# Kernel tuning notes

Measured on AMD Instinct MI355X. Metric: run time of the kernel, lower is better.

## Reference

```python
import jax, jax.numpy as jnp
import numpy as np

D_MODEL, D_STATE, D_CONV, EXPAND, L = 512, 16, 4, 2, 2048
D_INNER = EXPAND * D_MODEL


def _dwconv_causal(x, w, b):
    # x: (L, D), w: (D, K), b: (D,). torch Conv1d(groups=D, padding=K-1)[..., :L]
    K = w.shape[1]
    xp = jnp.pad(x, ((K - 1, 0), (0, 0)))
    windows = jnp.stack([xp[k:k + x.shape[0]] for k in range(K)], axis=-1)  # (L, D, K)
    return jnp.einsum('ldk,dk->ld', windows, w) + b


def _ssm_dir(x, inW, inb, cw, cb, xpW, xpb, dtW, dtb, outW, outb, A_log, Dp):
    xz = x @ inW + inb                      # (L, 2*Di)
    x_ssm, z = xz[:, :D_INNER], xz[:, D_INNER:]
    x_ssm = _dwconv_causal(x_ssm, cw, cb)   # (L, Di)
    sp = jax.nn.silu(x_ssm) @ xpW + xpb     # (L, Di + 2*S)
    delta = sp[:, :D_INNER]
    B = sp[:, D_INNER:D_INNER + D_STATE]
    C = sp[:, D_INNER + D_STATE:]
    dt = jax.nn.softplus(delta @ dtW + dtb)  # (L, Di)
    A = -jnp.exp(A_log)                      # (Di, S)
    dA = jnp.exp(dt[:, :, None] * A[None])                      # (L, Di, S)
    dBu = dt[:, :, None] * B[:, None, :] * x_ssm[:, :, None]    # (L, Di, S)

    def step(h, inp):
        a, bu = inp
        h = a * h + bu
        return h, h

    h0 = jnp.zeros((D_INNER, D_STATE), x.dtype)
    _, hs = jax.lax.scan(step, h0, (dA, dBu))   # (L, Di, S)
    y = jnp.einsum('lds,ls->ld', hs, C) + Dp * x_ssm
    return (y * jax.nn.silu(z)) @ outW + outb


def _make_params(key):
    ks = jax.random.split(key, 32)
    i = iter(range(32))
    def w(shape, scale=0.02):
        return (jax.random.normal(ks[next(i)], shape, jnp.float32) * scale)
    p = {}
    for pre in ('fwd_', 'bwd_'):
        p[pre + 'in_W'] = w((D_MODEL, 2 * D_INNER))
        p[pre + 'in_b'] = w((2 * D_INNER,))
        p[pre + 'conv_w'] = w((D_INNER, D_CONV), 0.1)
        p[pre + 'conv_b'] = w((D_INNER,))
        p[pre + 'xp_W'] = w((D_INNER, D_INNER + 2 * D_STATE))
        p[pre + 'xp_b'] = w((D_INNER + 2 * D_STATE,))
        p[pre + 'dt_W'] = w((D_INNER, D_INNER))
        p[pre + 'dt_b'] = w((D_INNER,))
        p[pre + 'out_W'] = w((D_INNER, D_MODEL))
        p[pre + 'out_b'] = w((D_MODEL,))
    p['A_log'] = jax.random.normal(ks[next(i)], (D_INNER, D_STATE), jnp.float32) * 0.5
    p['D_param'] = jnp.ones((D_INNER,), jnp.float32)
    p['fusion_W'] = w((2 * D_MODEL, D_MODEL))
    p['fusion_b'] = w((D_MODEL,))
    return p


def setup_inputs() -> dict:
    key = jax.random.key(0)
    kx, kp = jax.random.split(key)
    inp = {'x': jax.random.normal(kx, (L, D_MODEL), jnp.float32)}
    inp.update(_make_params(kp))
    return inp


def reference(x,
              fwd_in_W, fwd_in_b, fwd_conv_w, fwd_conv_b, fwd_xp_W, fwd_xp_b,
              fwd_dt_W, fwd_dt_b, fwd_out_W, fwd_out_b,
              bwd_in_W, bwd_in_b, bwd_conv_w, bwd_conv_b, bwd_xp_W, bwd_xp_b,
              bwd_dt_W, bwd_dt_b, bwd_out_W, bwd_out_b,
              A_log, D_param, fusion_W, fusion_b):
    out_fwd = _ssm_dir(x, fwd_in_W, fwd_in_b, fwd_conv_w, fwd_conv_b,
                       fwd_xp_W, fwd_xp_b, fwd_dt_W, fwd_dt_b,
                       fwd_out_W, fwd_out_b, A_log, D_param)
    out_bwd = _ssm_dir(x[::-1], bwd_in_W, bwd_in_b, bwd_conv_w, bwd_conv_b,
                       bwd_xp_W, bwd_xp_b, bwd_dt_W, bwd_dt_b,
                       bwd_out_W, bwd_out_b, A_log, D_param)[::-1]
    return jnp.concatenate([out_fwd, out_bwd], axis=-1) @ fusion_W + fusion_b
```

## Files before the change

### kernel.cpp

```cpp
#include <hip/hip_runtime.h>
#include <cmath>

#define L_SEQ 2048
#define DM 512
#define DI 1024
#define DS 16
#define NSP 1056
#define NC 64
#define CL 32

typedef unsigned short ushortT;
typedef unsigned int u32;
typedef __attribute__((ext_vector_type(8))) short short8;
typedef __attribute__((ext_vector_type(4))) float float4_t;
typedef __attribute__((address_space(1))) u32 gu32;
typedef __attribute__((address_space(3))) u32 lu32;

__device__ __forceinline__ float sigm(float x) { return 1.0f / (1.0f + __expf(-x)); }

__device__ __forceinline__ ushortT f2bf(float f) {
    unsigned u = __float_as_uint(f);
    unsigned r = u + 0x7FFFu + ((u >> 16) & 1u);
    return (ushortT)(r >> 16);
}

__device__ __forceinline__ void gl2lds16(const ushortT* g, ushortT* l) {
    __builtin_amdgcn_global_load_lds((gu32*)g, (lu32*)l, 16, 0, 0);
}

struct WC {
    const float* src[11];
    ushortT* dst[11];
    int ss[11], soff[11], ds_[11], tN[11], mode[11];
    int off[12];
};

__global__ __launch_bounds__(256) void wcvt_all(WC wc)
{
    __shared__ ushortT t[32][33];
    int b = blockIdx.x;
    int m = 0;
    while (b >= wc.off[m + 1]) ++m;
    int tl = b - wc.off[m];
    int n0 = (tl % wc.tN[m]) * 32;
    int k0 = (tl / wc.tN[m]) * 32;
    const float* W = wc.src[m];
    ushortT* D = wc.dst[m];
    int ss = wc.ss[m], soff = wc.soff[m], ds = wc.ds_[m];
    int tx = threadIdx.x & 31, ty = threadIdx.x >> 5;
    if (wc.mode[m] == 1) {
        #pragma unroll
        for (int i = 0; i < 32; i += 8)
            D[(size_t)(k0 + ty + i) * ds + n0 + tx] =
                f2bf(W[(size_t)(k0 + ty + i) * ss + soff + n0 + tx]);
    } else {
        #pragma unroll
        for (int i = 0; i < 32; i += 8)
            t[ty + i][tx] = f2bf(W[(size_t)(k0 + ty + i) * ss + soff + n0 + tx]);
        __syncthreads();
        #pragma unroll
        for (int i = 0; i < 32; i += 8)
            D[(size_t)(n0 + ty + i) * ds + k0 + tx] = t[tx][ty + i];
    }
}

__global__ __launch_bounds__(256) void bias_fold(
    const float* __restrict__ xpb0, const float* __restrict__ xpb1,
    const float* __restrict__ dtW0, const float* __restrict__ dtW1,
    const float* __restrict__ dtb0, const float* __restrict__ dtb1,
    const float* __restrict__ outb0, const float* __restrict__ outb1,
    const float* __restrict__ fuW, const float* __restrict__ fub,
    float* __restrict__ BFdt0, float* __restrict__ BFdt1, float* __restrict__ BFof)
{
    __shared__ float red[256];
    int o = blockIdx.x;
    int tid = threadIdx.x;
    float acc = 0.0f;
    if (o < 2112) {
        int dir = o >= 1056;
        int m = o - dir * 1056;
        const float* xpb = dir ? xpb1 : xpb0;
        float* BF = dir ? BFdt1 : BFdt0;
        if (m >= 1024) {
            if (tid == 0) BF[m] = xpb[m];
            return;
        }
        const float* dtW = dir ? dtW1 : dtW0;
        const float* dtb = dir ? dtb1 : dtb0;
        for (int n = tid; n < 1024; n += 256) acc += xpb[n] * dtW[n * 1024 + m];
        red[tid] = acc;
        __syncthreads();
        for (int s = 128; s > 0; s >>= 1) {
            if (tid < s) red[tid] += red[tid + s];
            __syncthreads();
        }
        if (tid == 0) BF[m] = red[0] + dtb[m];
    } else {
        int n = o - 2112;
        for (int j = tid; j < 1024; j += 256) {
            float ob = (j < 512) ? outb0[j] : outb1[j - 512];
            acc += ob * fuW[(size_t)j * 512 + n];
        }
        red[tid] = acc;
        __syncthreads();
        for (int s = 128; s > 0; s >>= 1) {
            if (tid < s) red[tid] += red[tid + s];
            __syncthreads();
        }
        if (tid == 0) BFof[n] = red[0] + fub[n];
    }
}

__global__ __launch_bounds__(256) void xcvt_k(const float* __restrict__ x,
                                              ushortT* __restrict__ xb, int n)
{
    int i = (blockIdx.x * 256 + threadIdx.x) * 4;
    if (i < n) {
        float4_t v = *(const float4_t*)(x + i);
        xb[i + 0] = f2bf(v[0]); xb[i + 1] = f2bf(v[1]);
        xb[i + 2] = f2bf(v[2]); xb[i + 3] = f2bf(v[3]);
    }
}

template<int BM, int BN>
__global__ __launch_bounds__(256) void gemm_bf16(
    const ushortT* __restrict__ A, int lda, long long Astr, int revAmode,
    const ushortT* __restrict__ W, long long Wstr,
    const float* __restrict__ bias0, const float* __restrict__ bias1,
    float* __restrict__ Cf, int ldcf, long long Cfstr,
    float* __restrict__ Cf2, int ldcf2, long long Cf2str, int Nsplit,
    ushortT* __restrict__ Cb, int ldcb, long long Cbstr,
    int M, int N, int K, int epi)
{
    const int dir = blockIdx.z;
    A  += (size_t)dir * Astr;
    W  += (size_t)dir * Wstr;
    if (Cf)  Cf  += (size_t)dir * Cfstr;
    if (Cf2) Cf2 += (size_t)dir * Cf2str;
    if (Cb)  Cb  += (size_t)dir * Cbstr;
    const float* bias = dir ? bias1 : bias0;
    const int revA = (revAmode == 2) ? dir : revAmode;

    constexpr int BK = 64;
    constexpr int MI = BM / 32;
    constexpr int NI = BN / 32;
    constexpr int CA = BM / 32;
    constexpr int CB = BN / 32;

    __shared__ ushortT As[2][BM * BK];
    __shared__ ushortT Bs[2][BN * BK];

    const int tid  = threadIdx.x;
    const int wave = tid >> 6;
    const int lane = tid & 63;
    const int quad = lane >> 4;
    const int r    = lane & 15;
    const int wm   = (wave >> 1) * (BM / 2);
    const int wn   = (wave & 1) * (BN / 2);
    const int bm   = blockIdx.y * BM;
    const int bn   = blockIdx.x * BN;

    const int lrow = lane >> 3;
    const int lk   = (lane & 7) * 8;

    const ushortT* gA[CA];
    ushortT* lA[CA];
    #pragma unroll
    for (int c = 0; c < CA; ++c) {
        int row = bm + c * 32 + wave * 8 + lrow;
        if (revA) row = M - 1 - row;
        gA[c] = A + (size_t)row * lda + lk;
        lA[c] = &As[0][(c * 32 + wave * 8) * BK];
    }
    const ushortT* gB[CB];
    ushortT* lB[CB];
    #pragma unroll
    for (int c = 0; c < CB; ++c) {
        int row = bn + c * 32 + wave * 8 + lrow;
        if (row > N - 1) row = N - 1;
        gB[c] = W + (size_t)row * K + lk;
        lB[c] = &Bs[0][(c * 32 + wave * 8) * BK];
    }
    constexpr int ABUF = BM * BK;
    constexpr int BBUF = BN * BK;

    float4_t acc[MI][NI];
    #pragma unroll
    for (int i = 0; i < MI; ++i)
        #pragma unroll
        for (int j = 0; j < NI; ++j)
            acc[i][j] = (float4_t){0.f, 0.f, 0.f, 0.f};

    const int nsteps = K >> 6;

    #pragma unroll
    for (int c = 0; c < CA; ++c) gl2lds16(gA[c], lA[c]);
    #pragma unroll
    for (int c = 0; c < CB; ++c) gl2lds16(gB[c], lB[c]);

    for (int i = 0; i < nsteps; i += 2) {
        __syncthreads();
        {
            int kq = (i + 1) << 6;
            if (i + 1 < nsteps) {
                #pragma unroll
                for (int c = 0; c < CA; ++c) gl2lds16(gA[c] + kq, lA[c] + ABUF);
                #pragma unroll
                for (int c = 0; c < CB; ++c) gl2lds16(gB[c] + kq, lB[c] + BBUF);
            }
        }
        #pragma unroll
        for (int kh = 0; kh < 2; ++kh) {
            short8 af[MI], bf[NI];
            #pragma unroll
            for (int mi = 0; mi < MI; ++mi)
                af[mi] = *(const short8*)&As[0][(wm + mi * 16 + r) * BK + kh * 32 + quad * 8];
            #pragma unroll
            for (int ni = 0; ni < NI; ++ni)
                bf[ni] = *(const short8*)&Bs[0][(wn + ni * 16 + r) * BK + kh * 32 + quad * 8];
            #pragma unroll
            for (int mi = 0; mi < MI; ++mi)
                #pragma unroll
                for (int ni = 0; ni < NI; ++ni)
                    acc[mi][ni] = __builtin_amdgcn_mfma_f32_16x16x32_bf16(
                        af[mi], bf[ni], acc[mi][ni], 0, 0, 0);
        }
        __syncthreads();
        {
            int kq = (i + 2) << 6;
            if (i + 2 < nsteps) {
                #pragma unroll
                for (int c = 0; c < CA; ++c) gl2lds16(gA[c] + kq, lA[c]);
                #pragma unroll
                for (int c = 0; c < CB; ++c) gl2lds16(gB[c] + kq, lB[c]);
            }
        }
        #pragma unroll
        for (int kh = 0; kh < 2; ++kh) {
            short8 af[MI], bf[NI];
            #pragma unroll
            for (int mi = 0; mi < MI; ++mi)
                af[mi] = *(const short8*)&As[1][(wm + mi * 16 + r) * BK + kh * 32 + quad * 8];
            #pragma unroll
            for (int ni = 0; ni < NI; ++ni)
                bf[ni] = *(const short8*)&Bs[1][(wn + ni * 16 + r) * BK + kh * 32 + quad * 8];
            #pragma unroll
            for (int mi = 0; mi < MI; ++mi)
                #pragma unroll
                for (int ni = 0; ni < NI; ++ni)
                    acc[mi][ni] = __builtin_amdgcn_mfma_f32_16x16x32_bf16(
                        af[mi], bf[ni], acc[mi][ni], 0, 0, 0);
        }
    }

    #pragma unroll
    for (int mi = 0; mi < MI; ++mi) {
        int rowb = bm + wm + mi * 16 + quad * 4;
        #pragma unroll
        for (int ni = 0; ni < NI; ++ni) {
            int gn = bn + wn + ni * 16 + r;
            if (gn < N) {
                float bv = bias ? bias[gn] : 0.0f;
                #pragma unroll
                for (int j = 0; j < 4; ++j) {
                    int orow = rowb + j;
                    float v = acc[mi][ni][j] + bv;
                    if (epi == 1 && gn < Nsplit) v = (v > 20.0f) ? v : log1pf(__expf(v));
                    if (epi == 3) {
                        atomicAdd(&Cf[(size_t)orow * ldcf + gn], v);
                    } else {
                        if (gn < Nsplit) {
                            if (Cf) Cf[(size_t)orow * ldcf + gn] = v;
                        } else if (Cf2) {
                            Cf2[(size_t)orow * ldcf2 + gn - Nsplit] = v;
                        }
                        if (Cb) Cb[(size_t)orow * ldcb + gn] = f2bf(v);
                    }
                }
            }
        }
    }
}

__global__ __launch_bounds__(256) void conv_k(
    const float* __restrict__ XZ,
    const float* __restrict__ cw0, const float* __restrict__ cw1,
    const float* __restrict__ cb0, const float* __restrict__ cb1,
    float* __restrict__ XC, ushortT* __restrict__ SCb)
{
    int dir = blockIdx.z;
    XZ += (size_t)dir * L_SEQ * 2 * DI;
    XC += (size_t)dir * L_SEQ * DI;
    SCb += (size_t)dir * L_SEQ * DI;
    const float* cw = dir ? cw1 : cw0;
    const float* cb = dir ? cb1 : cb0;
    int idx = blockIdx.x * 256 + threadIdx.x;
    int d = idx & (DI - 1);
    int l = idx >> 10;
    float w0 = cw[d * 4 + 0], w1 = cw[d * 4 + 1], w2 = cw[d * 4 + 2], w3 = cw[d * 4 + 3];
    float acc = cb[d];
    if (l >= 3) acc += XZ[(size_t)(l - 3) * (2 * DI) + d] * w0;
    if (l >= 2) acc += XZ[(size_t)(l - 2) * (2 * DI) + d] * w1;
    if (l >= 1) acc += XZ[(size_t)(l - 1) * (2 * DI) + d] * w2;
    acc += XZ[(size_t)l * (2 * DI) + d] * w3;
    XC[idx] = acc;
    SCb[idx] = f2bf(acc * sigm(acc));
}

__global__ __launch_bounds__(256) void scanA_k(
    const float* __restrict__ DT, const float* __restrict__ XC,
    const float* __restrict__ BC, const float* __restrict__ Alog,
    float* __restrict__ Pend, float* __restrict__ Hl)
{
    __shared__ float Bsh[CL][DS];
    int dir = blockIdx.z;
    int c = blockIdx.y;
    int d = blockIdx.x * 256 + threadIdx.x;
    DT += (size_t)dir * L_SEQ * DI;
    XC += (size_t)dir * L_SEQ * DI;
    BC += (size_t)dir * L_SEQ * 32;
    int l0 = c * CL;
    for (int i = threadIdx.x; i < CL * DS; i += 256) {
        int ll = i >> 4, ss = i & 15;
        Bsh[ll][ss] = BC[(size_t)(l0 + ll) * 32 + ss];
    }
    __syncthreads();
    float Ae[DS], h[DS], P[DS];
    #pragma unroll
    for (int s = 0; s < DS; ++s) { Ae[s] = -__expf(Alog[d * DS + s]); h[s] = 0.f; P[s] = 1.f; }
    for (int t = 0; t < CL; ++t) {
        int l = l0 + t;
        float dt = DT[(size_t)l * DI + d];
        float xv = XC[(size_t)l * DI + d];
        float dtx = dt * xv;
        #pragma unroll
        for (int s = 0; s < DS; ++s) {
            float e = __expf(dt * Ae[s]);
            h[s] = e * h[s] + dtx * Bsh[t][s];
            P[s] *= e;
        }
    }
    size_t o = ((size_t)(dir * NC + c) * DI + d) * DS;
    #pragma unroll
    for (int s = 0; s < DS; ++s) { Pend[o + s] = P[s]; Hl[o + s] = h[s]; }
}

__global__ __launch_bounds__(256) void scanB_k(
    const float* __restrict__ Pend, const float* __restrict__ Hl, float* __restrict__ Hs)
{
    int idx = blockIdx.x * 256 + threadIdx.x;
    float h = 0.f;
    int ds = idx & 16383;
    int dir = idx >> 14;
    for (int c = 0; c < NC; ++c) {
        size_t o = ((size_t)(dir * NC + c)) * (DI * DS) + ds;
        Hs[o] = h;
        h = Pend[o] * h + Hl[o];
    }
}

__global__ __launch_bounds__(256) void scanC_k(
    const float* __restrict__ DT, const float* __restrict__ XC,
    const float* __restrict__ BC, const float* __restrict__ XZ,
    const float* __restrict__ Alog, const float* __restrict__ Dp,
    const float* __restrict__ Hs, ushortT* __restrict__ Gb)
{
    __shared__ float Bsh[CL][DS];
    __shared__ float Csh[CL][DS];
    int dir = blockIdx.z;
    int c = blockIdx.y;
    int d = blockIdx.x * 256 + threadIdx.x;
    DT += (size_t)dir * L_SEQ * DI;
    XC += (size_t)dir * L_SEQ * DI;
    BC += (size_t)dir * L_SEQ * 32;
    XZ += (size_t)dir * L_SEQ * (2 * DI);
    Gb += (size_t)dir * L_SEQ * DI;
    int l0 = c * CL;
    for (int i = threadIdx.x; i < CL * DS; i += 256) {
        int ll = i >> 4, ss = i & 15;
        size_t base = (size_t)(l0 + ll) * 32;
        Bsh[ll][ss] = BC[base + ss];
        Csh[ll][ss] = BC[base + DS + ss];
    }
    __syncthreads();
    float Ae[DS], h[DS];
    size_t o = ((size_t)(dir * NC + c) * DI + d) * DS;
    #pragma unroll
    for (int s = 0; s < DS; ++s) { Ae[s] = -__expf(Alog[d * DS + s]); h[s] = Hs[o + s]; }
    float dpv = Dp[d];
    for (int t = 0; t < CL; ++t) {
        int l = l0 + t;
        float dt = DT[(size_t)l * DI + d];
        float xv = XC[(size_t)l * DI + d];
        float dtx = dt * xv;
        float y = 0.f;
        #pragma unroll
        for (int s = 0; s < DS; ++s) {
            float e = __expf(dt * Ae[s]);
            h[s] = e * h[s] + dtx * Bsh[t][s];
            y += h[s] * Csh[t][s];
        }
        y += dpv * xv;
        float z = XZ[(size_t)l * (2 * DI) + DI + d];
        Gb[(size_t)l * DI + d] = f2bf(y * (z * sigm(z)));
    }
}

extern "C" void kernel_launch(void* const* d_in, const int* in_sizes, int n_in,
                              void* d_out, int out_size, void* d_ws, size_t ws_size,
                              hipStream_t stream)
{
    (void)in_sizes; (void)n_in; (void)out_size; (void)ws_size;
    const float* x = (const float*)d_in[0];
    const float* inW[2]  = {(const float*)d_in[1],  (const float*)d_in[11]};
    const float* inb[2]  = {(const float*)d_in[2],  (const float*)d_in[12]};
    const float* cw[2]   = {(const float*)d_in[3],  (const float*)d_in[13]};
    const float* cb[2]   = {(const float*)d_in[4],  (const float*)d_in[14]};
    const float* xpW[2]  = {(const float*)d_in[5],  (const float*)d_in[15]};
    const float* xpb[2]  = {(const float*)d_in[6],  (const float*)d_in[16]};
    const float* dtW[2]  = {(const float*)d_in[7],  (const float*)d_in[17]};
    const float* dtb[2]  = {(const float*)d_in[8],  (const float*)d_in[18]};
    const float* outW[2] = {(const float*)d_in[9],  (const float*)d_in[19]};
    const float* outb[2] = {(const float*)d_in[10], (const float*)d_in[20]};
    const float* Alog = (const float*)d_in[21];
    const float* Dp   = (const float*)d_in[22];
    const float* fuW  = (const float*)d_in[23];
    const float* fub  = (const float*)d_in[24];
    float* out = (float*)d_out;

    float* ws = (float*)d_ws;
    size_t off = 0;
    auto alloc = [&](size_t n) { float* p = ws + off; off += n; return p; };
    float* XZ   = alloc((size_t)2 * L_SEQ * 2 * DI);
    float* XC   = alloc((size_t)2 * L_SEQ * DI);
    float* DTb  = alloc((size_t)2 * L_SEQ * DI);
    float* BCf  = alloc((size_t)2 * L_SEQ * 32);
    float* Pend = alloc((size_t)2 * NC * DI * DS);
    float* Hl   = alloc((size_t)2 * NC * DI * DS);
    float* Hs   = alloc((size_t)2 * NC * DI * DS);
    float* BFdt0 = alloc(1056);
    float* BFdt1 = alloc(1056);
    float* BFof  = alloc(512);

    ushortT* wsu = (ushortT*)(ws + off);
    size_t uoff = 0;
    auto ualloc = [&](size_t n) { ushortT* p = wsu + uoff; uoff += n; return p; };
    ushortT* WtIn  = ualloc((size_t)2 * (2 * DI) * DM);
    ushortT* WtDt  = ualloc((size_t)2 * DI * DI);
    ushortT* WtFu  = ualloc((size_t)DM * DI);
    ushortT* WtXpF = ualloc((size_t)2 * NSP * DI);
    ushortT* XpD   = ualloc((size_t)2 * DI * DI);
    ushortT* OutC  = ualloc((size_t)2 * DI * DM);
    ushortT* WtOF  = ualloc((size_t)2 * DM * DI);
    ushortT* XB    = ualloc((size_t)L_SEQ * DM);
    ushortT* SCb   = ualloc((size_t)2 * L_SEQ * DI);
    ushortT* Gb    = ualloc((size_t)2 * L_SEQ * DI);

    dim3 blk(256);

    hipMemsetAsync(out, 0, (size_t)L_SEQ * DM * sizeof(float), stream);

    WC wc;
    struct E { const float* s; ushortT* d; int ss, so, ds, N, K, mode; };
    E es[11] = {
        {inW[0],  WtIn,                          2 * DI, 0,    DM, 2 * DI, DM, 0},
        {inW[1],  WtIn + (size_t)2 * DI * DM,    2 * DI, 0,    DM, 2 * DI, DM, 0},
        {dtW[0],  WtDt,                          DI,     0,    DI, DI,     DI, 0},
        {dtW[1],  WtDt + (size_t)DI * DI,        DI,     0,    DI, DI,     DI, 0},
        {fuW,     WtFu,                          DM,     0,    DI, DM,     DI, 0},
        {xpW[0],  WtXpF + (size_t)DI * DI,       NSP,    DI,   DI, 32,     DI, 0},
        {xpW[1],  WtXpF + (size_t)NSP * DI + (size_t)DI * DI, NSP, DI, DI, 32, DI, 0},
        {xpW[0],  XpD,                           NSP,    0,    DI, DI,     DI, 1},
        {xpW[1],  XpD + (size_t)DI * DI,         NSP,    0,    DI, DI,     DI, 1},
        {outW[0], OutC,                          DM,     0,    DM, DM,     DI, 1},
        {outW[1], OutC + (size_t)DI * DM,        DM,     0,    DM, DM,     DI, 1},
    };
    wc.off[0] = 0;
    for (int m = 0; m < 11; ++m) {
        wc.src[m] = es[m].s; wc.dst[m] = es[m].d;
        wc.ss[m] = es[m].ss; wc.soff[m] = es[m].so; wc.ds_[m] = es[m].ds;
        wc.tN[m] = es[m].N / 32; wc.mode[m] = es[m].mode;
        wc.off[m + 1] = wc.off[m] + (es[m].N / 32) * (es[m].K / 32);
    }
    wcvt_all<<<dim3(wc.off[11]), blk, 0, stream>>>(wc);
    xcvt_k<<<dim3(L_SEQ * DM / 1024), blk, 0, stream>>>(x, XB, L_SEQ * DM);
    bias_fold<<<dim3(2624), blk, 0, stream>>>(
        xpb[0], xpb[1], dtW[0], dtW[1], dtb[0], dtb[1],
        outb[0], outb[1], fuW, fub, BFdt0, BFdt1, BFof);

    gemm_bf16<64, 64><<<dim3(16, 16, 2), blk, 0, stream>>>(
        WtDt, DI, (long long)DI * DI, 0, XpD, (long long)DI * DI,
        nullptr, nullptr, nullptr, 0, 0, nullptr, 0, 0, DI,
        WtXpF, DI, (long long)NSP * DI, DI, DI, DI, 0);
    gemm_bf16<64, 64><<<dim3(16, 8, 2), blk, 0, stream>>>(
        WtFu, DI, (long long)DM, 0, OutC, (long long)DI * DM,
        nullptr, nullptr, nullptr, 0, 0, nullptr, 0, 0, DI,
        WtOF, DI, (long long)DM * DI, DM, DI, DM, 0);

    gemm_bf16<64, 128><<<dim3(16, 32, 2), blk, 0, stream>>>(
        XB, DM, 0, 2, WtIn, (long long)2 * DI * DM, inb[0], inb[1],
        XZ, 2 * DI, (long long)L_SEQ * 2 * DI, nullptr, 0, 0, 2 * DI,
        nullptr, 0, 0, L_SEQ, 2 * DI, DM, 0);
    conv_k<<<dim3(L_SEQ * DI / 256, 1, 2), blk, 0, stream>>>(
        XZ, cw[0], cw[1], cb[0], cb[1], XC, SCb);
    gemm_bf16<64, 64><<<dim3((NSP + 63) / 64, 32, 2), blk, 0, stream>>>(
        SCb, DI, (long long)L_SEQ * DI, 0, WtXpF, (long long)NSP * DI, BFdt0, BFdt1,
        DTb, DI, (long long)L_SEQ * DI, BCf, 32, (long long)L_SEQ * 32, DI,
        nullptr, 0, 0, L_SEQ, NSP, DI, 1);
    scanA_k<<<dim3(DI / 256, NC, 2), blk, 0, stream>>>(DTb, XC, BCf, Alog, Pend, Hl);
    scanB_k<<<dim3(2 * DI * DS / 256), blk, 0, stream>>>(Pend, Hl, Hs);
    scanC_k<<<dim3(DI / 256, NC, 2), blk, 0, stream>>>(DTb, XC, BCf, XZ, Alog, Dp, Hs, Gb);
    gemm_bf16<64, 64><<<dim3(DM / 64, 32, 2), blk, 0, stream>>>(
        Gb, DI, (long long)L_SEQ * DI, 2, WtOF, (long long)DM * DI, BFof, nullptr,
        out, DM, 0, nullptr, 0, 0, DM,
        nullptr, 0, 0, L_SEQ, DM, DI, 3);
}
```

Before: 348.3 us.

## Merge prep kernels, swizzle LDS, fuse fold GEMMs, concat-K final GEMM without atomics

Merges weight conversion, input conversion and bias folding into one prep kernel, and merges the two weight-fold GEMMs into a single launch. An XOR swizzle is added to the LDS layout of the bf16 GEMM to cut bank conflicts. The final output GEMM now reads both directions as one concatenated K=2048 reduction (the backward half row-reversed), so the memset and atomicAdd epilogue are no longer needed. Tile shapes for the in-projection and x-projection GEMMs change to 128x64. The combined kernel reserves LDS for every block type, and each output block of the final GEMM now walks a longer K, leaving half as many blocks in flight.

After: 326.2 us. 6.3% less time.

```diff
diff --git a/kernel.cpp b/kernel.cpp
--- a/kernel.cpp
+++ b/kernel.cpp
@@ -35,36 +35,9 @@
     int off[12];
 };
 
-__global__ __launch_bounds__(256) void wcvt_all(WC wc)
-{
-    __shared__ ushortT t[32][33];
-    int b = blockIdx.x;
-    int m = 0;
-    while (b >= wc.off[m + 1]) ++m;
-    int tl = b - wc.off[m];
-    int n0 = (tl % wc.tN[m]) * 32;
-    int k0 = (tl / wc.tN[m]) * 32;
-    const float* W = wc.src[m];
-    ushortT* D = wc.dst[m];
-    int ss = wc.ss[m], soff = wc.soff[m], ds = wc.ds_[m];
-    int tx = threadIdx.x & 31, ty = threadIdx.x >> 5;
-    if (wc.mode[m] == 1) {
-        #pragma unroll
-        for (int i = 0; i < 32; i += 8)
-            D[(size_t)(k0 + ty + i) * ds + n0 + tx] =
-                f2bf(W[(size_t)(k0 + ty + i) * ss + soff + n0 + tx]);
-    } else {
-        #pragma unroll
-        for (int i = 0; i < 32; i += 8)
-            t[ty + i][tx] = f2bf(W[(size_t)(k0 + ty + i) * ss + soff + n0 + tx]);
-        __syncthreads();
-        #pragma unroll
-        for (int i = 0; i < 32; i += 8)
-            D[(size_t)(n0 + ty + i) * ds + k0 + tx] = t[tx][ty + i];
-    }
-}
-
-__global__ __launch_bounds__(256) void bias_fold(
+__global__ __launch_bounds__(256) void prep_all(
+    WC wc, int nW,
+    const float* __restrict__ x, ushortT* __restrict__ xb,
     const float* __restrict__ xpb0, const float* __restrict__ xpb1,
     const float* __restrict__ dtW0, const float* __restrict__ dtW1,
     const float* __restrict__ dtb0, const float* __restrict__ dtb1,
@@ -72,9 +45,45 @@
     const float* __restrict__ fuW, const float* __restrict__ fub,
     float* __restrict__ BFdt0, float* __restrict__ BFdt1, float* __restrict__ BFof)
 {
+    __shared__ ushortT t[32][33];
     __shared__ float red[256];
-    int o = blockIdx.x;
+    int b = blockIdx.x;
     int tid = threadIdx.x;
+    if (b < nW) {
+        int m = 0;
+        while (b >= wc.off[m + 1]) ++m;
+        int tl = b - wc.off[m];
+        int n0 = (tl % wc.tN[m]) * 32;
+        int k0 = (tl / wc.tN[m]) * 32;
+        const float* W = wc.src[m];
+        ushortT* D = wc.dst[m];
+        int ss = wc.ss[m], soff = wc.soff[m], ds = wc.ds_[m];
+        int tx = tid & 31, ty = tid >> 5;
+        if (wc.mode[m] == 1) {
+            #pragma unroll
+            for (int i = 0; i < 32; i += 8)
+                D[(size_t)(k0 + ty + i) * ds + n0 + tx] =
+                    f2bf(W[(size_t)(k0 + ty + i) * ss + soff + n0 + tx]);
+        } else {
+            #pragma unroll
+            for (int i = 0; i < 32; i += 8)
+                t[ty + i][tx] = f2bf(W[(size_t)(k0 + ty + i) * ss + soff + n0 + tx]);
+            __syncthreads();
+            #pragma unroll
+            for (int i = 0; i < 32; i += 8)
+                D[(size_t)(n0 + ty + i) * ds + k0 + tx] = t[tx][ty + i];
+        }
+        return;
+    }
+    b -= nW;
+    if (b < 1024) {
+        int i = (b * 256 + tid) * 4;
+        float4_t v = *(const float4_t*)(x + i);
+        xb[i + 0] = f2bf(v[0]); xb[i + 1] = f2bf(v[1]);
+        xb[i + 2] = f2bf(v[2]); xb[i + 3] = f2bf(v[3]);
+        return;
+    }
+    int o = b - 1024;
     float acc = 0.0f;
     if (o < 2112) {
         int dir = o >= 1056;
@@ -111,44 +120,25 @@
     }
 }
 
-__global__ __launch_bounds__(256) void xcvt_k(const float* __restrict__ x,
-                                              ushortT* __restrict__ xb, int n)
-{
-    int i = (blockIdx.x * 256 + threadIdx.x) * 4;
-    if (i < n) {
-        float4_t v = *(const float4_t*)(x + i);
-        xb[i + 0] = f2bf(v[0]); xb[i + 1] = f2bf(v[1]);
-        xb[i + 2] = f2bf(v[2]); xb[i + 3] = f2bf(v[3]);
-    }
-}
-
 template<int BM, int BN>
-__global__ __launch_bounds__(256) void gemm_bf16(
-    const ushortT* __restrict__ A, int lda, long long Astr, int revAmode,
-    const ushortT* __restrict__ W, long long Wstr,
-    const float* __restrict__ bias0, const float* __restrict__ bias1,
-    float* __restrict__ Cf, int ldcf, long long Cfstr,
-    float* __restrict__ Cf2, int ldcf2, long long Cf2str, int Nsplit,
-    ushortT* __restrict__ Cb, int ldcb, long long Cbstr,
+__device__ __forceinline__ void gemm_core(
+    ushortT* As, ushortT* Bs,
+    const ushortT* __restrict__ A, int lda, int revA,
+    const ushortT* __restrict__ A2, int dualK,
+    const ushortT* __restrict__ W,
+    const float* __restrict__ bias,
+    float* __restrict__ Cf, int ldcf,
+    float* __restrict__ Cf2, int ldcf2, int Nsplit,
+    ushortT* __restrict__ Cb, int ldcb,
     int M, int N, int K, int epi)
 {
-    const int dir = blockIdx.z;
-    A  += (size_t)dir * Astr;
-    W  += (size_t)dir * Wstr;
-    if (Cf)  Cf  += (size_t)dir * Cfstr;
-    if (Cf2) Cf2 += (size_t)dir * Cf2str;
-    if (Cb)  Cb  += (size_t)dir * Cbstr;
-    const float* bias = dir ? bias1 : bias0;
-    const int revA = (revAmode == 2) ? dir : revAmode;
-
     constexpr int BK = 64;
     constexpr int MI = BM / 32;
     constexpr int NI = BN / 32;
     constexpr int CA = BM / 32;
     constexpr int CB = BN / 32;
-
-    __shared__ ushortT As[2][BM * BK];
-    __shared__ ushortT Bs[2][BN * BK];
+    constexpr int ABUF = BM * BK;
+    constexpr int BBUF = BN * BK;
 
     const int tid  = threadIdx.x;
     const int wave = tid >> 6;
@@ -161,28 +151,25 @@
     const int bn   = blockIdx.x * BN;
 
     const int lrow = lane >> 3;
-    const int lk   = (lane & 7) * 8;
-
-    const ushortT* gA[CA];
-    ushortT* lA[CA];
+    const int lk   = ((lane & 7) ^ lrow) * 8;
+
+    const ushortT* gA[CA]; const ushortT* gA2[CA]; ushortT* lA[CA];
     #pragma unroll
     for (int c = 0; c < CA; ++c) {
         int row = bm + c * 32 + wave * 8 + lrow;
-        if (revA) row = M - 1 - row;
-        gA[c] = A + (size_t)row * lda + lk;
-        lA[c] = &As[0][(c * 32 + wave * 8) * BK];
-    }
-    const ushortT* gB[CB];
-    ushortT* lB[CB];
+        int r0 = revA ? (M - 1 - row) : row;
+        gA[c] = A + (size_t)r0 * lda + lk;
+        gA2[c] = dualK ? (A2 + (size_t)(M - 1 - row) * lda + lk) : gA[c];
+        lA[c] = &As[(c * 32 + wave * 8) * BK];
+    }
+    const ushortT* gB[CB]; ushortT* lB[CB];
     #pragma unroll
     for (int c = 0; c < CB; ++c) {
         int row = bn + c * 32 + wave * 8 + lrow;
         if (row > N - 1) row = N - 1;
         gB[c] = W + (size_t)row * K + lk;
-        lB[c] = &Bs[0][(c * 32 + wave * 8) * BK];
-    }
-    constexpr int ABUF = BM * BK;
-    constexpr int BBUF = BN * BK;
+        lB[c] = &Bs[(c * 32 + wave * 8) * BK];
+    }
 
     float4_t acc[MI][NI];
     #pragma unroll
@@ -193,31 +180,28 @@
 
     const int nsteps = K >> 6;
 
-    #pragma unroll
-    for (int c = 0; c < CA; ++c) gl2lds16(gA[c], lA[c]);
-    #pragma unroll
-    for (int c = 0; c < CB; ++c) gl2lds16(gB[c], lB[c]);
-
-    for (int i = 0; i < nsteps; i += 2) {
-        __syncthreads();
-        {
-            int kq = (i + 1) << 6;
-            if (i + 1 < nsteps) {
-                #pragma unroll
-                for (int c = 0; c < CA; ++c) gl2lds16(gA[c] + kq, lA[c] + ABUF);
-                #pragma unroll
-                for (int c = 0; c < CB; ++c) gl2lds16(gB[c] + kq, lB[c] + BBUF);
-            }
-        }
+    auto stage = [&](int step, int buf) {
+        int kq = step << 6;
+        #pragma unroll
+        for (int c = 0; c < CA; ++c) {
+            const ushortT* s = (!dualK || kq < 1024) ? gA[c] + kq : gA2[c] + (kq - 1024);
+            gl2lds16(s, lA[c] + buf * ABUF);
+        }
+        #pragma unroll
+        for (int c = 0; c < CB; ++c)
+            gl2lds16(gB[c] + kq, lB[c] + buf * BBUF);
+    };
+    auto compute = [&](int buf) {
         #pragma unroll
         for (int kh = 0; kh < 2; ++kh) {
+            const int slot = (((kh * 4 + quad) ^ (lane & 7)) * 8);
             short8 af[MI], bf[NI];
             #pragma unroll
             for (int mi = 0; mi < MI; ++mi)
-                af[mi] = *(const short8*)&As[0][(wm + mi * 16 + r) * BK + kh * 32 + quad * 8];
+                af[mi] = *(const short8*)&As[buf * ABUF + (wm + mi * 16 + r) * BK + slot];
             #pragma unroll
             for (int ni = 0; ni < NI; ++ni)
-                bf[ni] = *(const short8*)&Bs[0][(wn + ni * 16 + r) * BK + kh * 32 + quad * 8];
+                bf[ni] = *(const short8*)&Bs[buf * BBUF + (wn + ni * 16 + r) * BK + slot];
             #pragma unroll
             for (int mi = 0; mi < MI; ++mi)
                 #pragma unroll
@@ -225,32 +209,16 @@
                     acc[mi][ni] = __builtin_amdgcn_mfma_f32_16x16x32_bf16(
                         af[mi], bf[ni], acc[mi][ni], 0, 0, 0);
         }
+    };
+
+    stage(0, 0);
+    for (int i = 0; i < nsteps; i += 2) {
         __syncthreads();
-        {
-            int kq = (i + 2) << 6;
-            if (i + 2 < nsteps) {
-                #pragma unroll
-                for (int c = 0; c < CA; ++c) gl2lds16(gA[c] + kq, lA[c]);
-                #pragma unroll
-                for (int c = 0; c < CB; ++c) gl2lds16(gB[c] + kq, lB[c]);
-            }
-        }
-        #pragma unroll
-        for (int kh = 0; kh < 2; ++kh) {
-            short8 af[MI], bf[NI];
-            #pragma unroll
-            for (int mi = 0; mi < MI; ++mi)
-                af[mi] = *(const short8*)&As[1][(wm + mi * 16 + r) * BK + kh * 32 + quad * 8];
-            #pragma unroll
-            for (int ni = 0; ni < NI; ++ni)
-                bf[ni] = *(const short8*)&Bs[1][(wn + ni * 16 + r) * BK + kh * 32 + quad * 8];
-            #pragma unroll
-            for (int mi = 0; mi < MI; ++mi)
-                #pragma unroll
-                for (int ni = 0; ni < NI; ++ni)
-                    acc[mi][ni] = __builtin_amdgcn_mfma_f32_16x16x32_bf16(
-                        af[mi], bf[ni], acc[mi][ni], 0, 0, 0);
-        }
+        if (i + 1 < nsteps) stage(i + 1, 1);
+        compute(0);
+        __syncthreads();
+        if (i + 2 < nsteps) stage(i + 2, 0);
+        compute(1);
     }
 
     #pragma unroll
@@ -266,19 +234,69 @@
                     int orow = rowb + j;
                     float v = acc[mi][ni][j] + bv;
                     if (epi == 1 && gn < Nsplit) v = (v > 20.0f) ? v : log1pf(__expf(v));
-                    if (epi == 3) {
-                        atomicAdd(&Cf[(size_t)orow * ldcf + gn], v);
-                    } else {
-                        if (gn < Nsplit) {
-                            if (Cf) Cf[(size_t)orow * ldcf + gn] = v;
-                        } else if (Cf2) {
-                            Cf2[(size_t)orow * ldcf2 + gn - Nsplit] = v;
-                        }
-                        if (Cb) Cb[(size_t)orow * ldcb + gn] = f2bf(v);
+                    if (gn < Nsplit) {
+                        if (Cf) Cf[(size_t)orow * ldcf + gn] = v;
+                    } else if (Cf2) {
+                        Cf2[(size_t)orow * ldcf2 + gn - Nsplit] = v;
                     }
+                    if (Cb) Cb[(size_t)orow * ldcb + gn] = f2bf(v);
                 }
             }
         }
+    }
+}
+
+template<int BM, int BN>
+__global__ __launch_bounds__(256) void gemm_bf16(
+    const ushortT* __restrict__ A, int lda, long long Astr, int revAmode,
+    const ushortT* __restrict__ W, long long Wstr,
+    const float* __restrict__ bias0, const float* __restrict__ bias1,
+    float* __restrict__ Cf, int ldcf, long long Cfstr,
+    float* __restrict__ Cf2, int ldcf2, long long Cf2str, int Nsplit,
+    int M, int N, int K, int epi)
+{
+    __shared__ ushortT As[2 * BM * 64];
+    __shared__ ushortT Bs[2 * BN * 64];
+    const int dir = blockIdx.z;
+    const ushortT* Ad = A;
+    const ushortT* A2 = A;
+    int revA = 0, dualK = 0;
+    if (revAmode == 3) { dualK = 1; A2 = A + Astr; }
+    else { Ad += (size_t)dir * Astr; revA = (revAmode == 2) ? dir : revAmode; }
+    gemm_core<BM, BN>(As, Bs,
+        Ad, lda, revA, A2, dualK,
+        W + (size_t)dir * Wstr,
+        dir ? bias1 : bias0,
+        Cf ? Cf + (size_t)dir * Cfstr : nullptr, ldcf,
+        Cf2 ? Cf2 + (size_t)dir * Cf2str : nullptr, ldcf2, Nsplit,
+        nullptr, 0, M, N, K, epi);
+}
+
+__global__ __launch_bounds__(256) void gemm_fold(
+    const ushortT* __restrict__ WtDt, const ushortT* __restrict__ XpD,
+    ushortT* __restrict__ WtXpF,
+    const ushortT* __restrict__ WtFu, const ushortT* __restrict__ OutC,
+    ushortT* __restrict__ WtOF2)
+{
+    __shared__ ushortT As[2 * 64 * 64];
+    __shared__ ushortT Bs[2 * 64 * 64];
+    int z = blockIdx.z;
+    if (z < 2) {
+        gemm_core<64, 64>(As, Bs,
+            WtDt + (size_t)z * DI * DI, DI, 0, nullptr, 0,
+            XpD + (size_t)z * DI * DI,
+            nullptr, nullptr, 0, nullptr, 0, DI,
+            WtXpF + (size_t)z * NSP * DI, DI,
+            DI, DI, DI, 0);
+    } else {
+        if (blockIdx.y >= 8) return;
+        int d = z - 2;
+        gemm_core<64, 64>(As, Bs,
+            WtFu + (size_t)d * DM, DI, 0, nullptr, 0,
+            OutC + (size_t)d * DI * DM,
+            nullptr, nullptr, 0, nullptr, 0, DI,
+            WtOF2 + (size_t)d * DI, 2 * DI,
+            DM, DI, DM, 0);
     }
 }
 
@@ -451,14 +469,12 @@
     ushortT* WtXpF = ualloc((size_t)2 * NSP * DI);
     ushortT* XpD   = ualloc((size_t)2 * DI * DI);
     ushortT* OutC  = ualloc((size_t)2 * DI * DM);
-    ushortT* WtOF  = ualloc((size_t)2 * DM * DI);
+    ushortT* WtOF2 = ualloc((size_t)DM * 2 * DI);
     ushortT* XB    = ualloc((size_t)L_SEQ * DM);
     ushortT* SCb   = ualloc((size_t)2 * L_SEQ * DI);
     ushortT* Gb    = ualloc((size_t)2 * L_SEQ * DI);
 
     dim3 blk(256);
-
-    hipMemsetAsync(out, 0, (size_t)L_SEQ * DM * sizeof(float), stream);
 
     WC wc;
     struct E { const float* s; ushortT* d; int ss, so, ds, N, K, mode; };
@@ -482,36 +498,29 @@
         wc.tN[m] = es[m].N / 32; wc.mode[m] = es[m].mode;
         wc.off[m + 1] = wc.off[m] + (es[m].N / 32) * (es[m].K / 32);
     }
-    wcvt_all<<<dim3(wc.off[11]), blk, 0, stream>>>(wc);
-    xcvt_k<<<dim3(L_SEQ * DM / 1024), blk, 0, stream>>>(x, XB, L_SEQ * DM);
-    bias_fold<<<dim3(2624), blk, 0, stream>>>(
+    int nW = wc.off[11];
+    prep_all<<<dim3(nW + 1024 + 2624), blk, 0, stream>>>(
+        wc, nW, x, XB,
         xpb[0], xpb[1], dtW[0], dtW[1], dtb[0], dtb[1],
         outb[0], outb[1], fuW, fub, BFdt0, BFdt1, BFof);
 
-    gemm_bf16<64, 64><<<dim3(16, 16, 2), blk, 0, stream>>>(
-        WtDt, DI, (long long)DI * DI, 0, XpD, (long long)DI * DI,
-        nullptr, nullptr, nullptr, 0, 0, nullptr, 0, 0, DI,
-        WtXpF, DI, (long long)NSP * DI, DI, DI, DI, 0);
-    gemm_bf16<64, 64><<<dim3(16, 8, 2), blk, 0, stream>>>(
-        WtFu, DI, (long long)DM, 0, OutC, (long long)DI * DM,
-        nullptr, nullptr, nullptr, 0, 0, nullptr, 0, 0, DI,
-        WtOF, DI, (long long)DM * DI, DM, DI, DM, 0);
-
-    gemm_bf16<64, 128><<<dim3(16, 32, 2), blk, 0, stream>>>(
+    gemm_fold<<<dim3(16, 16, 4), blk, 0, stream>>>(WtDt, XpD, WtXpF, WtFu, OutC, WtOF2);
+
+    gemm_bf16<128, 64><<<dim3(32, 16, 2), blk, 0, stream>>>(
         XB, DM, 0, 2, WtIn, (long long)2 * DI * DM, inb[0], inb[1],
         XZ, 2 * DI, (long long)L_SEQ * 2 * DI, nullptr, 0, 0, 2 * DI,
-        nullptr, 0, 0, L_SEQ, 2 * DI, DM, 0);
+        L_SEQ, 2 * DI, DM, 0);
     conv_k<<<dim3(L_SEQ * DI / 256, 1, 2), blk, 0, stream>>>(
         XZ, cw[0], cw[1], cb[0], cb[1], XC, SCb);
-    gemm_bf16<64, 64><<<dim3((NSP + 63) / 64, 32, 2), blk, 0, stream>>>(
+    gemm_bf16<128, 64><<<dim3((NSP + 63) / 64, 16, 2), blk, 0, stream>>>(
         SCb, DI, (long long)L_SEQ * DI, 0, WtXpF, (long long)NSP * DI, BFdt0, BFdt1,
         DTb, DI, (long long)L_SEQ * DI, BCf, 32, (long long)L_SEQ * 32, DI,
-        nullptr, 0, 0, L_SEQ, NSP, DI, 1);
+        L_SEQ, NSP, DI, 1);
     scanA_k<<<dim3(DI / 256, NC, 2), blk, 0, stream>>>(DTb, XC, BCf, Alog, Pend, Hl);
     scanB_k<<<dim3(2 * DI * DS / 256), blk, 0, stream>>>(Pend, Hl, Hs);
     scanC_k<<<dim3(DI / 256, NC, 2), blk, 0, stream>>>(DTb, XC, BCf, XZ, Alog, Dp, Hs, Gb);
-    gemm_bf16<64, 64><<<dim3(DM / 64, 32, 2), blk, 0, stream>>>(
-        Gb, DI, (long long)L_SEQ * DI, 2, WtOF, (long long)DM * DI, BFof, nullptr,
+    gemm_bf16<64, 64><<<dim3(DM / 64, 32, 1), blk, 0, stream>>>(
+        Gb, DI, (long long)L_SEQ * DI, 3, WtOF2, 0, BFof, BFof,
         out, DM, 0, nullptr, 0, 0, DM,
-        nullptr, 0, 0, L_SEQ, DM, DI, 3);
-}
+        L_SEQ, DM, 2 * DI, 0);
+}
```
